# Kernel tuning notes

Hardware: AMD Instinct MI355X
Metric: run time of the kernel (lower is better)

The kernel has to match this reference:

```python
import jax, jax.numpy as jnp
import numpy as np

N_NODES, N_EDGES = 16384, 8192
IN_CH, HID_CH = 256, 256
ALPHA, BETA = -1.5, -0.5


def setup_inputs() -> dict:
    key = jax.random.key(0)
    k1, k2, k3, k4, k5, k6 = jax.random.split(key, 6)
    x_0 = jax.random.normal(k1, (N_NODES, IN_CH), dtype=jnp.float32)
    # binary incidence matrix (n_nodes, n_edges)
    incidence_1 = jax.random.randint(k2, (N_NODES, N_EDGES), 0, 2).astype(jnp.float32)
    # conv weights (torch Conv: x @ W then neighborhood @ .)
    W0 = jax.random.normal(k3, (IN_CH, HID_CH), dtype=jnp.float32) * 0.02
    W1 = jax.random.normal(k4, (HID_CH, HID_CH), dtype=jnp.float32) * 0.02
    # xavier_uniform biases of shape (1, hidden)
    gain = 1.414
    bound = gain * np.sqrt(6.0 / (1 + HID_CH)) * np.sqrt(3.0) / np.sqrt(3.0)  # xavier bound = gain*sqrt(6/(fan_in+fan_out))
    bound = gain * np.sqrt(6.0 / (1 + HID_CH))
    bias_0_to_1 = jax.random.uniform(k5, (1, HID_CH), minval=-bound, maxval=bound, dtype=jnp.float32)
    bias_1_to_0 = jax.random.uniform(k6, (1, HID_CH), minval=-bound, maxval=bound, dtype=jnp.float32)
    return {"x_0": x_0, "incidence_1": incidence_1, "W0": W0, "W1": W1,
            "bias_0_to_1": bias_0_to_1, "bias_1_to_0": bias_1_to_0}


def _normalize_incidence(B1):
    # edge/node cardinalities raised to alpha/beta
    edge_card = jnp.sum(B1, axis=0) ** ALPHA          # (n_edges,)
    node_card = jnp.sum(B1, axis=1) ** BETA           # (n_nodes,)
    mask = (B1 > 0).astype(B1.dtype)
    d0_inv = 1.0 / (mask @ edge_card)                 # (n_nodes,) per-node sum of incident edge_card
    d1_inv = 1.0 / (mask.T @ node_card)               # (n_edges,) per-edge sum of member node_card
    # B1_norm = D0_left^-1 @ B1 @ diag(edge_card)
    B1_norm = d0_inv[:, None] * B1 * edge_card[None, :]
    # B1T_norm = D1_left^-1 @ B1^T @ diag(node_card)
    B1T_norm = d1_inv[:, None] * B1.T * node_card[None, :]
    return B1_norm, B1T_norm


def reference(x_0, incidence_1, W0, W1, bias_0_to_1, bias_1_to_0):
    B1_norm, B1T_norm = _normalize_incidence(incidence_1)
    # node -> edge conv: x_1 = B1T_norm @ (x_0 @ W0) + b01
    x_1 = B1T_norm @ (x_0 @ W0) + bias_0_to_1        # (n_edges, hid)
    # edge -> node conv: x_0 = B1_norm @ (x_1 @ W1) + b10
    x_0_out = B1_norm @ (x_1 @ W1) + bias_1_to_0     # (n_nodes, hid)
    return jax.nn.relu(x_0_out), jax.nn.relu(x_1)
```

## Files before the change

### kernel.cpp

```cpp
#include <hip/hip_runtime.h>
#include <stdint.h>

#define NN 16384
#define NE 8192
#define CH 256
#define MM1_SPLIT 8
#define MM2_SPLIT 4

typedef __attribute__((ext_vector_type(8))) short bf16x8;
typedef __attribute__((ext_vector_type(4))) float f32x4;

__device__ __forceinline__ unsigned short f2bf(float f) {
  unsigned u = __float_as_uint(f);
  u += 0x7FFFu + ((u >> 16) & 1u);
  return (unsigned short)(u >> 16);
}
__device__ __forceinline__ void async_copy16(const void* gptr, void* lptr) {
  __builtin_amdgcn_global_load_lds((const __attribute__((address_space(1))) unsigned int*)gptr,
                                   (__attribute__((address_space(3))) unsigned int*)lptr,
                                   16, 0, 0);
}
__device__ __forceinline__ uint4 expand8(unsigned byte) {
  uint4 aw;
#pragma unroll
  for (int j = 0; j < 4; ++j) {
    unsigned lo = (byte >> (2 * j)) & 1u;
    unsigned hi = (byte >> (2 * j + 1)) & 1u;
    ((unsigned*)&aw)[j] = lo * 0x3F80u + hi * 0x3F800000u;
  }
  return aw;
}

__device__ __forceinline__ void transpose32(unsigned* x) {
  const unsigned masks[5] = {0x0000FFFFu, 0x00FF00FFu, 0x0F0F0F0Fu, 0x33333333u, 0x55555555u};
#pragma unroll
  for (int jj = 0; jj < 5; ++jj) {
    const int j = 16 >> jj;
    const unsigned m = masks[jj];
#pragma unroll
    for (int k = 0; k < 32; ++k) {
      if ((k & j) == 0) {
        unsigned t = ((x[k] >> j) ^ x[k + j]) & m;
        x[k] ^= (t << j);
        x[k + j] ^= t;
      }
    }
  }
}

__global__ void k0_transpose_w(const float* __restrict__ W0, const float* __restrict__ W1,
                               unsigned short* __restrict__ W0T, unsigned short* __restrict__ W1T) {
  const float* W = blockIdx.y ? W1 : W0;
  unsigned short* WT = blockIdx.y ? W1T : W0T;
  int n = blockIdx.x;
  int k = threadIdx.x;
  WT[n * CH + k] = f2bf(W[k * CH + n]);
}

__global__ void k1_pack_card(const float* __restrict__ B1, unsigned* __restrict__ pk1,
                             float* __restrict__ node_card) {
  int n = blockIdx.x;
  int t = threadIdx.x;
  const float4* p = (const float4*)(B1 + (size_t)n * NE + t * 32);
  unsigned w = 0;
#pragma unroll
  for (int jj = 0; jj < 8; ++jj) {
    float4 v = p[jj];
    w |= ((__float_as_uint(v.x) >> 23) & 1u) << (4 * jj);
    w |= ((__float_as_uint(v.y) >> 23) & 1u) << (4 * jj + 1);
    w |= ((__float_as_uint(v.z) >> 23) & 1u) << (4 * jj + 2);
    w |= ((__float_as_uint(v.w) >> 23) & 1u) << (4 * jj + 3);
  }
  pk1[(size_t)n * 256 + t] = w;
  int s = __popc(w);
  __shared__ int red[4];
#pragma unroll
  for (int off = 32; off; off >>= 1) s += __shfl_down(s, off, 64);
  if ((t & 63) == 0) red[t >> 6] = s;
  __syncthreads();
  if (t == 0) {
    float tot = (float)(red[0] + red[1] + red[2] + red[3]);
    node_card[n] = rsqrtf(tot);
  }
}

__global__ __launch_bounds__(256) void k1b_bitT(const unsigned* __restrict__ pk1,
                                                unsigned* __restrict__ pk1T) {
  int bw = blockIdx.x & 127;
  int half = blockIdx.x >> 7;
  int t = threadIdx.x;
  int nt = half * 256 + t;
  unsigned x0[32], x1[32];
#pragma unroll
  for (int r = 0; r < 32; ++r) {
    uint2 v = *(const uint2*)&pk1[(size_t)(nt * 32 + r) * 256 + 2 * bw];
    x0[r] = v.x;
    x1[r] = v.y;
  }
  transpose32(x0);
  transpose32(x1);
  int e0 = bw * 64;
#pragma unroll
  for (int c = 0; c < 32; ++c) {
    pk1T[(size_t)(e0 + c) * 512 + nt] = x0[c];
    pk1T[(size_t)(e0 + 32 + c) * 512 + nt] = x1[c];
  }
}

__global__ __launch_bounds__(256) void ke_edge(const unsigned* __restrict__ pk1T,
                                               const float* __restrict__ node_card,
                                               float* __restrict__ edge_card,
                                               float* __restrict__ d1) {
  const int t = threadIdx.x;
  const int e0 = blockIdx.x * 4;
  unsigned w[4][2];
#pragma unroll
  for (int r = 0; r < 4; ++r) {
    w[r][0] = pk1T[(size_t)(e0 + r) * 512 + t];
    w[r][1] = pk1T[(size_t)(e0 + r) * 512 + 256 + t];
  }
  float wsum[4] = {0.f, 0.f, 0.f, 0.f};
  int cnt[4];
#pragma unroll
  for (int r = 0; r < 4; ++r) cnt[r] = __popc(w[r][0]) + __popc(w[r][1]);
  const float4* nc0 = (const float4*)(node_card + (size_t)t * 32);
  const float4* nc1 = (const float4*)(node_card + ((size_t)t + 256) * 32);
#pragma unroll
  for (int h = 0; h < 2; ++h) {
    const float4* ncp = h ? nc1 : nc0;
#pragma unroll
    for (int q = 0; q < 8; ++q) {
      float4 v = ncp[q];
#pragma unroll
      for (int r = 0; r < 4; ++r) {
        unsigned ww = w[r][h];
        wsum[r] += ((ww >> (4 * q)) & 1u) ? v.x : 0.f;
        wsum[r] += ((ww >> (4 * q + 1)) & 1u) ? v.y : 0.f;
        wsum[r] += ((ww >> (4 * q + 2)) & 1u) ? v.z : 0.f;
        wsum[r] += ((ww >> (4 * q + 3)) & 1u) ? v.w : 0.f;
      }
    }
  }
#pragma unroll
  for (int off = 32; off; off >>= 1)
#pragma unroll
    for (int r = 0; r < 4; ++r) {
      wsum[r] += __shfl_down(wsum[r], off, 64);
      cnt[r] += __shfl_down(cnt[r], off, 64);
    }
  __shared__ float redW[4][4];
  __shared__ int redC[4][4];
  int wave = t >> 6, lane = t & 63;
  if (lane == 0)
#pragma unroll
    for (int r = 0; r < 4; ++r) {
      redW[wave][r] = wsum[r];
      redC[wave][r] = cnt[r];
    }
  __syncthreads();
  if (t < 4) {
    float s = redW[0][t] + redW[1][t] + redW[2][t] + redW[3][t];
    float c = (float)(redC[0][t] + redC[1][t] + redC[2][t] + redC[3][t]);
    d1[e0 + t] = s;
    edge_card[e0 + t] = 1.0f / (c * sqrtf(c));
  }
}

__global__ __launch_bounds__(256) void kd0_node(const unsigned* __restrict__ pk1,
                                                const float* __restrict__ edge_card,
                                                float* __restrict__ d0) {
  const int t = threadIdx.x;
  const int n0 = blockIdx.x * 4;
  unsigned w[4];
#pragma unroll
  for (int r = 0; r < 4; ++r) w[r] = pk1[(size_t)(n0 + r) * 256 + t];
  float wsum[4] = {0.f, 0.f, 0.f, 0.f};
  const float4* ecp = (const float4*)(edge_card + (size_t)t * 32);
#pragma unroll
  for (int q = 0; q < 8; ++q) {
    float4 v = ecp[q];
#pragma unroll
    for (int r = 0; r < 4; ++r) {
      unsigned ww = w[r];
      wsum[r] += ((ww >> (4 * q)) & 1u) ? v.x : 0.f;
      wsum[r] += ((ww >> (4 * q + 1)) & 1u) ? v.y : 0.f;
      wsum[r] += ((ww >> (4 * q + 2)) & 1u) ? v.z : 0.f;
      wsum[r] += ((ww >> (4 * q + 3)) & 1u) ? v.w : 0.f;
    }
  }
#pragma unroll
  for (int off = 32; off; off >>= 1)
#pragma unroll
    for (int r = 0; r < 4; ++r) wsum[r] += __shfl_down(wsum[r], off, 64);
  __shared__ float redW[4][4];
  int wave = t >> 6, lane = t & 63;
  if (lane == 0)
#pragma unroll
    for (int r = 0; r < 4; ++r) redW[wave][r] = wsum[r];
  __syncthreads();
  if (t < 4) d0[n0 + t] = redW[0][t] + redW[1][t] + redW[2][t] + redW[3][t];
}

__global__ __launch_bounds__(256) void k2_y0(const float* __restrict__ X0,
                                             const unsigned short* __restrict__ W0T,
                                             const float* __restrict__ node_card,
                                             unsigned short* __restrict__ y0sT) {
  __shared__ __align__(16) unsigned short a_lds[32 * 32];
  __shared__ __align__(16) unsigned short b_lds[256 * 32];
  const int tid = threadIdx.x;
  const int wave = tid >> 6, lane = tid & 63;
  const int quad = lane >> 4, l15 = lane & 15;
  const int m0 = blockIdx.x * 32;
  const int ar = tid >> 3, ac = (tid & 7) * 4;

  f32x4 acc[2][4];
  const f32x4 fz = {0.f, 0.f, 0.f, 0.f};
#pragma unroll
  for (int i = 0; i < 2; ++i)
#pragma unroll
    for (int j = 0; j < 4; ++j) acc[i][j] = fz;

  for (int k0 = 0; k0 < CH; k0 += 32) {
    __syncthreads();
    {
      float4 v = *(const float4*)(X0 + (size_t)(m0 + ar) * CH + k0 + ac);
      uint2 w;
      w.x = ((unsigned)f2bf(v.x)) | ((unsigned)f2bf(v.y) << 16);
      w.y = ((unsigned)f2bf(v.z)) | ((unsigned)f2bf(v.w) << 16);
      *(uint2*)&a_lds[ar * 32 + ac] = w;
    }
#pragma unroll
    for (int i = 0; i < 4; ++i) {
      int rowbase = wave * 64 + i * 16;
      const unsigned short* g = W0T + (size_t)(rowbase + (lane >> 2)) * CH + k0 + (lane & 3) * 8;
      async_copy16(g, &b_lds[rowbase * 32]);
    }
    __syncthreads();
    bf16x8 af[2];
#pragma unroll
    for (int i = 0; i < 2; ++i)
      af[i] = *(const bf16x8*)&a_lds[(i * 16 + l15) * 32 + quad * 8];
#pragma unroll
    for (int j = 0; j < 4; ++j) {
      bf16x8 bfr = *(const bf16x8*)&b_lds[(wave * 64 + j * 16 + l15) * 32 + quad * 8];
#pragma unroll
      for (int i = 0; i < 2; ++i)
        acc[i][j] = __builtin_amdgcn_mfma_f32_16x16x32_bf16(af[i], bfr, acc[i][j], 0, 0, 0);
    }
  }
#pragma unroll
  for (int i = 0; i < 2; ++i) {
    int row4 = m0 + i * 16 + quad * 4;
    float4 nc = *(const float4*)(node_card + row4);
#pragma unroll
    for (int j = 0; j < 4; ++j) {
      int col = wave * 64 + j * 16 + l15;
      f32x4 v = acc[i][j];
      ushort4 o;
      o.x = f2bf(v[0] * nc.x);
      o.y = f2bf(v[1] * nc.y);
      o.z = f2bf(v[2] * nc.z);
      o.w = f2bf(v[3] * nc.w);
      *(ushort4*)&y0sT[(size_t)col * NN + row4] = o;
    }
  }
}

__global__ __launch_bounds__(512, 4) void mm1_kernel(const unsigned char* __restrict__ pk1T,
                                                     const unsigned short* __restrict__ y0sT,
                                                     float* __restrict__ mm1p) {
  __shared__ __align__(16) unsigned short a_lds[2][128 * 40];
  __shared__ __align__(16) unsigned short b_lds[2][256 * 32];
  const int tid = threadIdx.x;
  const int wave = tid >> 6, lane = tid & 63;
  const int quad = lane >> 4, l15 = lane & 15;
  const int wm = wave >> 2, wn = wave & 3;
  const int bid = blockIdx.x;
  const int sp = bid & 7;
  const int m0 = (bid >> 3) * 128;
  const int KS = NN / MM1_SPLIT;
  const int NT = KS / 32;
  const int kbase = sp * KS;

  const int am = tid >> 2;
  const int akg = tid & 3;
  const int ajbs = akg ^ ((am >> 4) & 3);
  const int aoff = am * 40 + ajbs * 8;
  const int brow = lane >> 2;
  const int bcol = (lane & 3) * 8;

  f32x4 acc[4][4];
  const f32x4 fz = {0.f, 0.f, 0.f, 0.f};
#pragma unroll
  for (int i = 0; i < 4; ++i)
#pragma unroll
    for (int j = 0; j < 4; ++j) acc[i][j] = fz;

  const unsigned char* agp = pk1T + (size_t)(m0 + am) * (NN / 8) + (kbase >> 3) + akg;
  unsigned ab_cur = agp[0];
  unsigned ab_nxt = agp[4];
  const unsigned char* agq = agp + 8;

#pragma unroll
  for (int i = 0; i < 2; ++i) {
    int rowbase = wave * 32 + i * 16;
    const unsigned short* g = y0sT + (size_t)(rowbase + brow) * NN + kbase + bcol;
    async_copy16(g, &b_lds[0][rowbase * 32]);
  }
  *(uint4*)&a_lds[0][aoff] = expand8(ab_cur);
  __syncthreads();

  for (int t = 0; t < NT; ++t) {
    const int cur = t & 1;
    unsigned ab_new = 0;
    if (t + 1 < NT) {
      const int k0n = kbase + (t + 1) * 32;
#pragma unroll
      for (int i = 0; i < 2; ++i) {
        int rowbase = wave * 32 + i * 16;
        const unsigned short* g = y0sT + (size_t)(rowbase + brow) * NN + k0n + bcol;
        async_copy16(g, &b_lds[cur ^ 1][rowbase * 32]);
      }
      *(uint4*)&a_lds[cur ^ 1][aoff] = expand8(ab_nxt);
      if (t + 2 < NT) {
        ab_new = *agq;
        agq += 4;
      }
    }
    bf16x8 af[4];
#pragma unroll
    for (int i = 0; i < 4; ++i) {
      int m = wm * 64 + i * 16 + l15;
      int jbs = quad ^ ((m >> 4) & 3);
      af[i] = *(const bf16x8*)&a_lds[cur][m * 40 + jbs * 8];
    }
#pragma unroll
    for (int j = 0; j < 4; ++j) {
      bf16x8 bfr = *(const bf16x8*)&b_lds[cur][(wn * 64 + j * 16 + l15) * 32 + quad * 8];
#pragma unroll
      for (int i = 0; i < 4; ++i)
        acc[i][j] = __builtin_amdgcn_mfma_f32_16x16x32_bf16(af[i], bfr, acc[i][j], 0, 0, 0);
    }
    __syncthreads();
    ab_cur = ab_nxt;
    ab_nxt = ab_new;
  }
  float* outp = mm1p + (size_t)sp * NE * CH;
#pragma unroll
  for (int i = 0; i < 4; ++i) {
    int row4 = m0 + wm * 64 + i * 16 + quad * 4;
#pragma unroll
    for (int j = 0; j < 4; ++j) {
      int col = wn * 64 + j * 16 + l15;
#pragma unroll
      for (int r = 0; r < 4; ++r) outp[(size_t)(row4 + r) * CH + col] = acc[i][j][r];
    }
  }
}

__global__ void k3_edge_final(const float* __restrict__ mm1p, const float* __restrict__ d1,
                              const float* __restrict__ b01,
                              float* __restrict__ out1, unsigned short* __restrict__ x1bf) {
  int e = blockIdx.x, c = threadIdx.x;
  float p = 0.f;
#pragma unroll
  for (int sp = 0; sp < MM1_SPLIT; ++sp)
    p += mm1p[(size_t)sp * NE * CH + (size_t)e * CH + c];
  float x1 = p / d1[e] + b01[c];
  out1[(size_t)e * CH + c] = fmaxf(x1, 0.f);
  x1bf[(size_t)e * CH + c] = f2bf(x1);
}

__global__ __launch_bounds__(256) void k5_y1(const unsigned short* __restrict__ x1bf,
                                             const unsigned short* __restrict__ W1T,
                                             const float* __restrict__ edge_card,
                                             unsigned short* __restrict__ y1sT) {
  __shared__ __align__(16) unsigned short a_lds[32 * 32];
  __shared__ __align__(16) unsigned short b_lds[256 * 32];
  const int tid = threadIdx.x;
  const int wave = tid >> 6, lane = tid & 63;
  const int quad = lane >> 4, l15 = lane & 15;
  const int m0 = blockIdx.x * 32;

  f32x4 acc[2][4];
  const f32x4 fz = {0.f, 0.f, 0.f, 0.f};
#pragma unroll
  for (int i = 0; i < 2; ++i)
#pragma unroll
    for (int j = 0; j < 4; ++j) acc[i][j] = fz;

  for (int k0 = 0; k0 < CH; k0 += 32) {
    __syncthreads();
    if (wave < 2) {
      const unsigned short* g = x1bf + (size_t)(m0 + wave * 16 + (lane >> 2)) * CH + k0 + (lane & 3) * 8;
      async_copy16(g, &a_lds[(wave * 16) * 32]);
    }
#pragma unroll
    for (int i = 0; i < 4; ++i) {
      int rowbase = wave * 64 + i * 16;
      const unsigned short* g = W1T + (size_t)(rowbase + (lane >> 2)) * CH + k0 + (lane & 3) * 8;
      async_copy16(g, &b_lds[rowbase * 32]);
    }
    __syncthreads();
    bf16x8 af[2];
#pragma unroll
    for (int i = 0; i < 2; ++i)
      af[i] = *(const bf16x8*)&a_lds[(i * 16 + l15) * 32 + quad * 8];
#pragma unroll
    for (int j = 0; j < 4; ++j) {
      bf16x8 bfr = *(const bf16x8*)&b_lds[(wave * 64 + j * 16 + l15) * 32 + quad * 8];
#pragma unroll
      for (int i = 0; i < 2; ++i)
        acc[i][j] = __builtin_amdgcn_mfma_f32_16x16x32_bf16(af[i], bfr, acc[i][j], 0, 0, 0);
    }
  }
#pragma unroll
  for (int i = 0; i < 2; ++i) {
    int row4 = m0 + i * 16 + quad * 4;
    float4 ec = *(const float4*)(edge_card + row4);
#pragma unroll
    for (int j = 0; j < 4; ++j) {
      int col = wave * 64 + j * 16 + l15;
      f32x4 v = acc[i][j];
      ushort4 o;
      o.x = f2bf(v[0] * ec.x);
      o.y = f2bf(v[1] * ec.y);
      o.z = f2bf(v[2] * ec.z);
      o.w = f2bf(v[3] * ec.w);
      *(ushort4*)&y1sT[(size_t)col * NE + row4] = o;
    }
  }
}

__global__ __launch_bounds__(512, 4) void mm2_kernel(const unsigned char* __restrict__ pk1,
                                                     const unsigned short* __restrict__ y1sT,
                                                     float* __restrict__ mm2p) {
  __shared__ __align__(16) unsigned short a_lds[2][128 * 40];
  __shared__ __align__(16) unsigned short b_lds[2][256 * 32];
  const int tid = threadIdx.x;
  const int wave = tid >> 6, lane = tid & 63;
  const int quad = lane >> 4, l15 = lane & 15;
  const int wm = wave >> 2, wn = wave & 3;
  const int bid = blockIdx.x;
  const int sp = (bid >> 1) & 3;
  const int m0 = (((bid >> 3) << 1) | (bid & 1)) * 128;
  const int KS = NE / MM2_SPLIT;
  const int NT = KS / 32;
  const int kbase = sp * KS;

  const int am = tid >> 2;
  const int akg = tid & 3;
  const int ajbs = akg ^ ((am >> 4) & 3);
  const int aoff = am * 40 + ajbs * 8;
  const int brow = lane >> 2;
  const int bcol = (lane & 3) * 8;

  f32x4 acc[4][4];
  const f32x4 fz = {0.f, 0.f, 0.f, 0.f};
#pragma unroll
  for (int i = 0; i < 4; ++i)
#pragma unroll
    for (int j = 0; j < 4; ++j) acc[i][j] = fz;

  const unsigned char* agp = pk1 + (size_t)(m0 + am) * (NE / 8) + (kbase >> 3) + akg;
  unsigned ab_cur = agp[0];
  unsigned ab_nxt = agp[4];
  const unsigned char* agq = agp + 8;

#pragma unroll
  for (int i = 0; i < 2; ++i) {
    int rowbase = wave * 32 + i * 16;
    const unsigned short* g = y1sT + (size_t)(rowbase + brow) * NE + kbase + bcol;
    async_copy16(g, &b_lds[0][rowbase * 32]);
  }
  *(uint4*)&a_lds[0][aoff] = expand8(ab_cur);
  __syncthreads();

  for (int t = 0; t < NT; ++t) {
    const int cur = t & 1;
    unsigned ab_new = 0;
    if (t + 1 < NT) {
      const int k0n = kbase + (t + 1) * 32;
#pragma unroll
      for (int i = 0; i < 2; ++i) {
        int rowbase = wave * 32 + i * 16;
        const unsigned short* g = y1sT + (size_t)(rowbase + brow) * NE + k0n + bcol;
        async_copy16(g, &b_lds[cur ^ 1][rowbase * 32]);
      }
      *(uint4*)&a_lds[cur ^ 1][aoff] = expand8(ab_nxt);
      if (t + 2 < NT) {
        ab_new = *agq;
        agq += 4;
      }
    }
    bf16x8 af[4];
#pragma unroll
    for (int i = 0; i < 4; ++i) {
      int m = wm * 64 + i * 16 + l15;
      int jbs = quad ^ ((m >> 4) & 3);
      af[i] = *(const bf16x8*)&a_lds[cur][m * 40 + jbs * 8];
    }
#pragma unroll
    for (int j = 0; j < 4; ++j) {
      bf16x8 bfr = *(const bf16x8*)&b_lds[cur][(wn * 64 + j * 16 + l15) * 32 + quad * 8];
#pragma unroll
      for (int i = 0; i < 4; ++i)
        acc[i][j] = __builtin_amdgcn_mfma_f32_16x16x32_bf16(af[i], bfr, acc[i][j], 0, 0, 0);
    }
    __syncthreads();
    ab_cur = ab_nxt;
    ab_nxt = ab_new;
  }
  float* outp = mm2p + (size_t)sp * NN * CH;
#pragma unroll
  for (int i = 0; i < 4; ++i) {
    int row4 = m0 + wm * 64 + i * 16 + quad * 4;
#pragma unroll
    for (int j = 0; j < 4; ++j) {
      int col = wn * 64 + j * 16 + l15;
#pragma unroll
      for (int r = 0; r < 4; ++r) outp[(size_t)(row4 + r) * CH + col] = acc[i][j][r];
    }
  }
}

__global__ void k6_node_final(const float* __restrict__ mm2p, const float* __restrict__ d0,
                              const float* __restrict__ b10, float* __restrict__ out0) {
  int n = blockIdx.x, c = threadIdx.x;
  float s = 0.f;
#pragma unroll
  for (int sp = 0; sp < MM2_SPLIT; ++sp)
    s += mm2p[(size_t)sp * NN * CH + (size_t)n * CH + c];
  float v = s / d0[n] + b10[c];
  out0[(size_t)n * CH + c] = fmaxf(v, 0.f);
}

extern "C" void kernel_launch(void* const* d_in, const int* in_sizes, int n_in,
                              void* d_out, int out_size, void* d_ws, size_t ws_size,
                              hipStream_t stream) {
  const float* x0 = (const float*)d_in[0];
  const float* B1 = (const float*)d_in[1];
  const float* W0 = (const float*)d_in[2];
  const float* W1 = (const float*)d_in[3];
  const float* b01 = (const float*)d_in[4];
  const float* b10 = (const float*)d_in[5];
  float* out0 = (float*)d_out;
  float* out1 = out0 + (size_t)NN * CH;

  char* ws = (char*)d_ws;
  size_t off = 0;
  auto take = [&](size_t bytes) {
    void* p = ws + off;
    off += (bytes + 255) & ~(size_t)255;
    return p;
  };
  unsigned short* y0sT = (unsigned short*)take((size_t)256 * NN * 2);
  unsigned short* y1sT = (unsigned short*)take((size_t)256 * NE * 2);
  unsigned short* x1bf = (unsigned short*)take((size_t)NE * CH * 2);
  float* mm1p = (float*)take((size_t)MM1_SPLIT * NE * CH * 4);
  float* mm2p = mm1p;
  float* node_card = (float*)take((size_t)NN * 4);
  float* edge_card = (float*)take((size_t)NE * 4);
  float* d1 = (float*)take((size_t)NE * 4);
  float* d0 = (float*)take((size_t)NN * 4);
  unsigned short* W0T = (unsigned short*)take((size_t)CH * CH * 2);
  unsigned short* W1T = (unsigned short*)take((size_t)CH * CH * 2);
  unsigned* pk1 = (unsigned*)take((size_t)NN * 256 * 4);
  unsigned* pk1T = (unsigned*)take((size_t)NE * 512 * 4);
  (void)ws_size; (void)in_sizes; (void)n_in; (void)out_size;

  k0_transpose_w<<<dim3(256, 2), 256, 0, stream>>>(W0, W1, W0T, W1T);
  k1_pack_card<<<NN, 256, 0, stream>>>(B1, pk1, node_card);
  k1b_bitT<<<256, 256, 0, stream>>>(pk1, pk1T);
  ke_edge<<<NE / 4, 256, 0, stream>>>(pk1T, node_card, edge_card, d1);
  kd0_node<<<NN / 4, 256, 0, stream>>>(pk1, edge_card, d0);
  k2_y0<<<NN / 32, 256, 0, stream>>>(x0, W0T, node_card, y0sT);
  mm1_kernel<<<512, 512, 0, stream>>>((const unsigned char*)pk1T, y0sT, mm1p);
  k3_edge_final<<<NE, 256, 0, stream>>>(mm1p, d1, b01, out1, x1bf);
  k5_y1<<<NE / 32, 256, 0, stream>>>(x1bf, W1T, edge_card, y1sT);
  mm2_kernel<<<512, 512, 0, stream>>>((const unsigned char*)pk1, y1sT, mm2p);
  k6_node_final<<<NN, 256, 0, stream>>>(mm2p, d0, b10, out0);
}
```

Before: 956.0 us.

## Expand bit-packed incidence directly into MFMA registers, skip LDS staging; vectorize finalizers

The mm1 and mm2 GEMMs no longer stage the expanded A tile (bit-packed incidence turned into bf16) through shared memory. Each lane loads the bytes it needs for its own MFMA fragments from global memory and expands them in registers. This removes the A-side LDS writes and reads and part of the LDS footprint, at the cost of redundant byte loads across the four wn waves and less latency hiding for those loads. It also raises wave priority around the MFMA block, and it vectorizes the split-K reduction kernels to float4, with four rows per block and a reciprocal multiply.

```diff
diff --git a/kernel.cpp b/kernel.cpp
--- a/kernel.cpp
+++ b/kernel.cpp
@@ -269,7 +269,6 @@
 __global__ __launch_bounds__(512, 4) void mm1_kernel(const unsigned char* __restrict__ pk1T,
                                                      const unsigned short* __restrict__ y0sT,
                                                      float* __restrict__ mm1p) {
-  __shared__ __align__(16) unsigned short a_lds[2][128 * 40];
   __shared__ __align__(16) unsigned short b_lds[2][256 * 32];
   const int tid = threadIdx.x;
   const int wave = tid >> 6, lane = tid & 63;
@@ -281,11 +280,8 @@
   const int KS = NN / MM1_SPLIT;
   const int NT = KS / 32;
   const int kbase = sp * KS;
-
-  const int am = tid >> 2;
-  const int akg = tid & 3;
-  const int ajbs = akg ^ ((am >> 4) & 3);
-  const int aoff = am * 40 + ajbs * 8;
+  const int AST = NN / 8;
+
   const int brow = lane >> 2;
   const int bcol = (lane & 3) * 8;
 
@@ -296,10 +292,10 @@
 #pragma unroll
     for (int j = 0; j < 4; ++j) acc[i][j] = fz;
 
-  const unsigned char* agp = pk1T + (size_t)(m0 + am) * (NN / 8) + (kbase >> 3) + akg;
-  unsigned ab_cur = agp[0];
-  unsigned ab_nxt = agp[4];
-  const unsigned char* agq = agp + 8;
+  const unsigned char* abase = pk1T + (size_t)(m0 + wm * 64 + l15) * AST + (kbase >> 3) + quad;
+  unsigned ab[4];
+#pragma unroll
+  for (int i = 0; i < 4; ++i) ab[i] = abase[(size_t)(i * 16) * AST];
 
 #pragma unroll
   for (int i = 0; i < 2; ++i) {
@@ -307,12 +303,10 @@
     const unsigned short* g = y0sT + (size_t)(rowbase + brow) * NN + kbase + bcol;
     async_copy16(g, &b_lds[0][rowbase * 32]);
   }
-  *(uint4*)&a_lds[0][aoff] = expand8(ab_cur);
   __syncthreads();
 
   for (int t = 0; t < NT; ++t) {
     const int cur = t & 1;
-    unsigned ab_new = 0;
     if (t + 1 < NT) {
       const int k0n = kbase + (t + 1) * 32;
 #pragma unroll
@@ -321,19 +315,18 @@
         const unsigned short* g = y0sT + (size_t)(rowbase + brow) * NN + k0n + bcol;
         async_copy16(g, &b_lds[cur ^ 1][rowbase * 32]);
       }
-      *(uint4*)&a_lds[cur ^ 1][aoff] = expand8(ab_nxt);
-      if (t + 2 < NT) {
-        ab_new = *agq;
-        agq += 4;
-      }
     }
     bf16x8 af[4];
 #pragma unroll
     for (int i = 0; i < 4; ++i) {
-      int m = wm * 64 + i * 16 + l15;
-      int jbs = quad ^ ((m >> 4) & 3);
-      af[i] = *(const bf16x8*)&a_lds[cur][m * 40 + jbs * 8];
-    }
+      uint4 ue = expand8(ab[i]);
+      af[i] = *reinterpret_cast<bf16x8*>(&ue);
+    }
+    if (t + 1 < NT) {
+#pragma unroll
+      for (int i = 0; i < 4; ++i) ab[i] = abase[(size_t)(i * 16) * AST + (t + 1) * 4];
+    }
+    __builtin_amdgcn_s_setprio(1);
 #pragma unroll
     for (int j = 0; j < 4; ++j) {
       bf16x8 bfr = *(const bf16x8*)&b_lds[cur][(wn * 64 + j * 16 + l15) * 32 + quad * 8];
@@ -341,9 +334,8 @@
       for (int i = 0; i < 4; ++i)
         acc[i][j] = __builtin_amdgcn_mfma_f32_16x16x32_bf16(af[i], bfr, acc[i][j], 0, 0, 0);
     }
+    __builtin_amdgcn_s_setprio(0);
     __syncthreads();
-    ab_cur = ab_nxt;
-    ab_nxt = ab_new;
   }
   float* outp = mm1p + (size_t)sp * NE * CH;
 #pragma unroll
@@ -358,17 +350,34 @@
   }
 }
 
-__global__ void k3_edge_final(const float* __restrict__ mm1p, const float* __restrict__ d1,
-                              const float* __restrict__ b01,
-                              float* __restrict__ out1, unsigned short* __restrict__ x1bf) {
-  int e = blockIdx.x, c = threadIdx.x;
-  float p = 0.f;
-#pragma unroll
-  for (int sp = 0; sp < MM1_SPLIT; ++sp)
-    p += mm1p[(size_t)sp * NE * CH + (size_t)e * CH + c];
-  float x1 = p / d1[e] + b01[c];
-  out1[(size_t)e * CH + c] = fmaxf(x1, 0.f);
-  x1bf[(size_t)e * CH + c] = f2bf(x1);
+__global__ __launch_bounds__(256) void k3_edge_final(const float* __restrict__ mm1p,
+                                                     const float* __restrict__ d1,
+                                                     const float* __restrict__ b01,
+                                                     float* __restrict__ out1,
+                                                     unsigned short* __restrict__ x1bf) {
+  const int t = threadIdx.x;
+  const int e = blockIdx.x * 4 + (t >> 6);
+  const int c4 = (t & 63) * 4;
+  float px = 0.f, py = 0.f, pz = 0.f, pw = 0.f;
+#pragma unroll
+  for (int sp = 0; sp < MM1_SPLIT; ++sp) {
+    float4 v = *(const float4*)&mm1p[(size_t)sp * NE * CH + (size_t)e * CH + c4];
+    px += v.x; py += v.y; pz += v.z; pw += v.w;
+  }
+  const float rd = 1.0f / d1[e];
+  const float4 b = *(const float4*)&b01[c4];
+  float4 x1;
+  x1.x = px * rd + b.x;
+  x1.y = py * rd + b.y;
+  x1.z = pz * rd + b.z;
+  x1.w = pw * rd + b.w;
+  float4 o;
+  o.x = fmaxf(x1.x, 0.f); o.y = fmaxf(x1.y, 0.f);
+  o.z = fmaxf(x1.z, 0.f); o.w = fmaxf(x1.w, 0.f);
+  *(float4*)&out1[(size_t)e * CH + c4] = o;
+  ushort4 xb;
+  xb.x = f2bf(x1.x); xb.y = f2bf(x1.y); xb.z = f2bf(x1.z); xb.w = f2bf(x1.w);
+  *(ushort4*)&x1bf[(size_t)e * CH + c4] = xb;
 }
 
 __global__ __launch_bounds__(256) void k5_y1(const unsigned short* __restrict__ x1bf,
@@ -435,7 +444,6 @@
 __global__ __launch_bounds__(512, 4) void mm2_kernel(const unsigned char* __restrict__ pk1,
                                                      const unsigned short* __restrict__ y1sT,
                                                      float* __restrict__ mm2p) {
-  __shared__ __align__(16) unsigned short a_lds[2][128 * 40];
   __shared__ __align__(16) unsigned short b_lds[2][256 * 32];
   const int tid = threadIdx.x;
   const int wave = tid >> 6, lane = tid & 63;
@@ -447,11 +455,8 @@
   const int KS = NE / MM2_SPLIT;
   const int NT = KS / 32;
   const int kbase = sp * KS;
-
-  const int am = tid >> 2;
-  const int akg = tid & 3;
-  const int ajbs = akg ^ ((am >> 4) & 3);
-  const int aoff = am * 40 + ajbs * 8;
+  const int AST = NE / 8;
+
   const int brow = lane >> 2;
   const int bcol = (lane & 3) * 8;
 
@@ -462,10 +467,10 @@
 #pragma unroll
     for (int j = 0; j < 4; ++j) acc[i][j] = fz;
 
-  const unsigned char* agp = pk1 + (size_t)(m0 + am) * (NE / 8) + (kbase >> 3) + akg;
-  unsigned ab_cur = agp[0];
-  unsigned ab_nxt = agp[4];
-  const unsigned char* agq = agp + 8;
+  const unsigned char* abase = pk1 + (size_t)(m0 + wm * 64 + l15) * AST + (kbase >> 3) + quad;
+  unsigned ab[4];
+#pragma unroll
+  for (int i = 0; i < 4; ++i) ab[i] = abase[(size_t)(i * 16) * AST];
 
 #pragma unroll
   for (int i = 0; i < 2; ++i) {
@@ -473,12 +478,10 @@
     const unsigned short* g = y1sT + (size_t)(rowbase + brow) * NE + kbase + bcol;
     async_copy16(g, &b_lds[0][rowbase * 32]);
   }
-  *(uint4*)&a_lds[0][aoff] = expand8(ab_cur);
   __syncthreads();
 
   for (int t = 0; t < NT; ++t) {
     const int cur = t & 1;
-    unsigned ab_new = 0;
     if (t + 1 < NT) {
       const int k0n = kbase + (t + 1) * 32;
 #pragma unroll
@@ -487,19 +490,18 @@
         const unsigned short* g = y1sT + (size_t)(rowbase + brow) * NE + k0n + bcol;
         async_copy16(g, &b_lds[cur ^ 1][rowbase * 32]);
       }
-      *(uint4*)&a_lds[cur ^ 1][aoff] = expand8(ab_nxt);
-      if (t + 2 < NT) {
-        ab_new = *agq;
-        agq += 4;
-      }
     }
     bf16x8 af[4];
 #pragma unroll
     for (int i = 0; i < 4; ++i) {
-      int m = wm * 64 + i * 16 + l15;
-      int jbs = quad ^ ((m >> 4) & 3);
-      af[i] = *(const bf16x8*)&a_lds[cur][m * 40 + jbs * 8];
-    }
+      uint4 ue = expand8(ab[i]);
+      af[i] = *reinterpret_cast<bf16x8*>(&ue);
+    }
+    if (t + 1 < NT) {
+#pragma unroll
+      for (int i = 0; i < 4; ++i) ab[i] = abase[(size_t)(i * 16) * AST + (t + 1) * 4];
+    }
+    __builtin_amdgcn_s_setprio(1);
 #pragma unroll
     for (int j = 0; j < 4; ++j) {
       bf16x8 bfr = *(const bf16x8*)&b_lds[cur][(wn * 64 + j * 16 + l15) * 32 + quad * 8];
@@ -507,9 +509,8 @@
       for (int i = 0; i < 4; ++i)
         acc[i][j] = __builtin_amdgcn_mfma_f32_16x16x32_bf16(af[i], bfr, acc[i][j], 0, 0, 0);
     }
+    __builtin_amdgcn_s_setprio(0);
     __syncthreads();
-    ab_cur = ab_nxt;
-    ab_nxt = ab_new;
   }
   float* outp = mm2p + (size_t)sp * NN * CH;
 #pragma unroll
@@ -524,15 +525,27 @@
   }
 }
 
-__global__ void k6_node_final(const float* __restrict__ mm2p, const float* __restrict__ d0,
-                              const float* __restrict__ b10, float* __restrict__ out0) {
-  int n = blockIdx.x, c = threadIdx.x;
-  float s = 0.f;
-#pragma unroll
-  for (int sp = 0; sp < MM2_SPLIT; ++sp)
-    s += mm2p[(size_t)sp * NN * CH + (size_t)n * CH + c];
-  float v = s / d0[n] + b10[c];
-  out0[(size_t)n * CH + c] = fmaxf(v, 0.f);
+__global__ __launch_bounds__(256) void k6_node_final(const float* __restrict__ mm2p,
+                                                     const float* __restrict__ d0,
+                                                     const float* __restrict__ b10,
+                                                     float* __restrict__ out0) {
+  const int t = threadIdx.x;
+  const int n = blockIdx.x * 4 + (t >> 6);
+  const int c4 = (t & 63) * 4;
+  float sx = 0.f, sy = 0.f, sz = 0.f, sw = 0.f;
+#pragma unroll
+  for (int sp = 0; sp < MM2_SPLIT; ++sp) {
+    float4 v = *(const float4*)&mm2p[(size_t)sp * NN * CH + (size_t)n * CH + c4];
+    sx += v.x; sy += v.y; sz += v.z; sw += v.w;
+  }
+  const float rd = 1.0f / d0[n];
+  const float4 b = *(const float4*)&b10[c4];
+  float4 o;
+  o.x = fmaxf(sx * rd + b.x, 0.f);
+  o.y = fmaxf(sy * rd + b.y, 0.f);
+  o.z = fmaxf(sz * rd + b.z, 0.f);
+  o.w = fmaxf(sw * rd + b.w, 0.f);
+  *(float4*)&out0[(size_t)n * CH + c4] = o;
 }
 
 extern "C" void kernel_launch(void* const* d_in, const int* in_sizes, int n_in,
@@ -576,8 +589,8 @@
   kd0_node<<<NN / 4, 256, 0, stream>>>(pk1, edge_card, d0);
   k2_y0<<<NN / 32, 256, 0, stream>>>(x0, W0T, node_card, y0sT);
   mm1_kernel<<<512, 512, 0, stream>>>((const unsigned char*)pk1T, y0sT, mm1p);
-  k3_edge_final<<<NE, 256, 0, stream>>>(mm1p, d1, b01, out1, x1bf);
+  k3_edge_final<<<NE / 4, 256, 0, stream>>>(mm1p, d1, b01, out1, x1bf);
   k5_y1<<<NE / 32, 256, 0, stream>>>(x1bf, W1T, edge_card, y1sT);
   mm2_kernel<<<512, 512, 0, stream>>>((const unsigned char*)pk1, y1sT, mm2p);
-  k6_node_final<<<NN, 256, 0, stream>>>(mm2p, d0, b10, out0);
-}
+  k6_node_final<<<NN / 4, 256, 0, stream>>>(mm2p, d0, b10, out0);
+}
```

Measured after the change: 1.122 ms. 17.3% more time.
